# Kernel tuning notes

Measured on AMD Instinct MI355X. Metric: run time of the kernel, lower is better.

The kernel has to match this reference:

```python
import jax, jax.numpy as jnp
import numpy as np

H = 100
N = 262144

def setup_inputs() -> dict:
    key = jax.random.key(0)
    ks = jax.random.split(key, 9)
    s = 1.0 / np.sqrt(H)
    return {
        "m": jax.random.normal(ks[0], (1, H), jnp.float32),
        "output_hidden": jax.random.normal(ks[1], (1, 1, H), jnp.float32),
        "fact_embeddings": jax.random.normal(ks[2], (N, H), jnp.float32),
        "W1": jax.random.normal(ks[3], (H, 2 * H), jnp.float32) * s,
        "b1": jax.random.normal(ks[4], (H,), jnp.float32) * s,
        "W2": jax.random.normal(ks[5], (1, H), jnp.float32) * s,
        "b2": jax.random.normal(ks[6], (1,), jnp.float32) * s,
        "W3": jax.random.normal(ks[7], (H, 3 * H), jnp.float32) * s,
        "b3": jax.random.normal(ks[8], (H,), jnp.float32) * s,
    }

def reference(m, output_hidden, fact_embeddings, W1, b1, W2, b2, W3, b3):
    output_context = output_hidden[0]                      # [1, H]
    # z = [|f - oh| ; |f - m|]  -> [N, 2H] (broadcast over N)
    z = jnp.concatenate(
        [jnp.abs(fact_embeddings - output_context),
         jnp.abs(fact_embeddings - m)], axis=1)
    # MLP attention scores, softmax over N facts
    g = jnp.tanh(z @ W1.T + b1) @ W2.T + b2                # [N, 1]
    g = jax.nn.softmax(g.ravel())                          # [N]
    # Weighted-sum pooling of facts
    c = (g[:, None] * fact_embeddings).sum(axis=0, keepdims=True)  # [1, H]
    # Gated memory update
    m_new = jax.nn.relu(jnp.concatenate([m, c, output_context], axis=1) @ W3.T + b3)
    return m_new
```

## Files before the change

kernel.cpp:

```cpp
#include <hip/hip_runtime.h>
#include <hip/hip_bf16.h>
#include <math.h>

#define HDIM 100
#define NFACT 262144
#define FPB   128
#define NBLK_T 2048
#define TPB   4
#define GRID  (NBLK_T / TPB)
#define NTHREADS 512

#define KHALF 112
#define NJT 7
#define NKC 7
#define NBFRAG (NJT * NKC * 64)

#define NCOPY 116
#define NSTRIPE 4

using short8 = __attribute__((ext_vector_type(8))) short;
using f32x4  = __attribute__((ext_vector_type(4))) float;

#define WS_B    0
#define WS_ACC  12544

__device__ __forceinline__ unsigned short f2bf(float x) {
    unsigned u = __builtin_bit_cast(unsigned, x);
    u += 0x7FFFu + ((u >> 16) & 1u);
    return (unsigned short)(u >> 16);
}

__device__ __forceinline__ float tanh_fast(float x) {
    float e = __expf(2.0f * x);
    return 1.0f - 2.0f / (1.0f + e);
}

__global__ __launch_bounds__(256) void k_prep_b(const float* __restrict__ W1,
                                                float* __restrict__ ws) {
    int tg = blockIdx.x * 256 + threadIdx.x;
    if (tg < NSTRIPE * NCOPY) ws[WS_ACC + tg] = 0.f;
    if (tg >= NBFRAG) return;
    int lane = tg & 63;
    int kc = (tg >> 6) % NKC;
    int jt = tg / (NKC * 64);
    int g = lane >> 4, r = lane & 15;
    int j = jt * 16 + r;
    unsigned short v[8];
    #pragma unroll
    for (int e = 0; e < 8; e++) {
        int kglob = kc * 32 + g * 8 + e;
        int half = (kglob >= KHALF) ? 1 : 0;
        int koff = kglob - half * KHALF;
        float x = 0.f;
        if (j < HDIM && koff < HDIM) x = W1[j * 200 + half * HDIM + koff];
        v[e] = f2bf(x);
    }
    uint4 d;
    d.x = (unsigned)v[0] | ((unsigned)v[1] << 16);
    d.y = (unsigned)v[2] | ((unsigned)v[3] << 16);
    d.z = (unsigned)v[4] | ((unsigned)v[5] << 16);
    d.w = (unsigned)v[6] | ((unsigned)v[7] << 16);
    ((uint4*)(ws + WS_B))[tg] = d;
}

__device__ __forceinline__ float4 ld4c(const float* p, bool ok) {
    float4 z = make_float4(0.f, 0.f, 0.f, 0.f);
    return ok ? *(const float4*)p : z;
}

__device__ __forceinline__ uint4 pack_absdiff_u(float4 a0, float4 a1,
                                                float4 b0, float4 b1) {
    union { __hip_bfloat16 h[8]; uint4 u; } u;
    u.h[0] = __float2bfloat16(fabsf(a0.x - b0.x));
    u.h[1] = __float2bfloat16(fabsf(a0.y - b0.y));
    u.h[2] = __float2bfloat16(fabsf(a0.z - b0.z));
    u.h[3] = __float2bfloat16(fabsf(a0.w - b0.w));
    u.h[4] = __float2bfloat16(fabsf(a1.x - b1.x));
    u.h[5] = __float2bfloat16(fabsf(a1.y - b1.y));
    u.h[6] = __float2bfloat16(fabsf(a1.z - b1.z));
    u.h[7] = __float2bfloat16(fabsf(a1.w - b1.w));
    return u.u;
}

__device__ __forceinline__ float4 shfl32_f4(float4 v) {
    float4 r;
    r.x = __shfl_xor(v.x, 32); r.y = __shfl_xor(v.y, 32);
    r.z = __shfl_xor(v.z, 32); r.w = __shfl_xor(v.w, 32);
    return r;
}

template<int CTRL>
__device__ __forceinline__ float dpp_radd(float x) {
    int y = __builtin_amdgcn_update_dpp(0, __builtin_bit_cast(int, x),
                                        CTRL, 0xF, 0xF, true);
    return x + __builtin_bit_cast(float, y);
}
__device__ __forceinline__ float row_reduce16(float x) {
    x = dpp_radd<0x121>(x);
    x = dpp_radd<0x122>(x);
    x = dpp_radd<0x124>(x);
    x = dpp_radd<0x128>(x);
    return x;
}

__global__ __launch_bounds__(NTHREADS, 2) void k_logits(
        const float* __restrict__ fe,
        const float* __restrict__ oc,
        const float* __restrict__ mvec,
        const float* __restrict__ b1,
        const float* __restrict__ W2,
        float* __restrict__ ws) {
    __shared__ __align__(16) uint4 Bs[NBFRAG];
    __shared__ float poolS[KHALF];
    __shared__ float cpad[2 * KHALF];
    __shared__ float bw[2 * KHALF];
    __shared__ float sS;

    int t = threadIdx.x;
    int w = t >> 6, lane = t & 63, g = lane >> 4, r = lane & 15;
    bool ghi = (lane & 32) != 0;

    if (t == 0) sS = 0.f;
    if (t < KHALF) poolS[t] = 0.f;

    if (t < 2 * KHALF) {
        int half = t / KHALF, k = t % KHALF;
        cpad[t] = (k < HDIM) ? (half ? mvec[k] : oc[k]) : 0.f;
        bw[t]   = (k < HDIM) ? (half ? W2[k]   : b1[k]) : 0.f;
    }

    {
        const uint4* Bg = (const uint4*)(ws + WS_B);
        #pragma unroll
        for (int i = 0; i < 7; i++) {
            int base = i * 512 + w * 64;
            if (base < NBFRAG) {
                __builtin_amdgcn_global_load_lds(
                    (const __attribute__((address_space(1))) unsigned int*)(Bg + base + lane),
                    (__attribute__((address_space(3))) unsigned int*)(Bs + base),
                    16, 0, 0);
            }
        }
    }

    int row_off = w * 16 + r;

    auto issue_load = [&](int tile, float4* f0, float4* f1) {
        const float* fp = fe + ((long)tile * FPB + row_off) * HDIM;
        if (tile != NBLK_T - 1) {
            #pragma unroll
            for (int kc = 0; kc < 4; kc++) {
                int pk = kc * 32 + g * 8;
                int col = (pk >= KHALF) ? (pk - KHALF) : pk;
                f0[kc] = *(const float4*)(fp + col);
                f1[kc] = *(const float4*)(fp + col + 4);
            }
        } else {
            #pragma unroll
            for (int kc = 0; kc < 4; kc++) {
                int pk = kc * 32 + g * 8;
                int col = (pk >= KHALF) ? (pk - KHALF) : pk;
                f0[kc] = ld4c(fp + col, col < HDIM);
                f1[kc] = ld4c(fp + col + 4, col + 4 < HDIM);
            }
        }
    };

    float sacc = 0.f;

    auto process = [&](float4* f0c, float4* f1c) {
        uint4 zabs[NKC];
        #pragma unroll
        for (int kc = 0; kc < 4; kc++) {
            int pk = kc * 32 + g * 8;
            float4 s0 = *(const float4*)(cpad + pk);
            float4 s1 = *(const float4*)(cpad + pk + 4);
            zabs[kc] = pack_absdiff_u(f0c[kc], f1c[kc], s0, s1);
        }
        #pragma unroll
        for (int c = 0; c < 3; c++) {
            int pk = (4 + c) * 32 + g * 8;
            float4 sa0 = ghi ? f0c[c] : f0c[c + 1];
            float4 sa1 = ghi ? f1c[c] : f1c[c + 1];
            float4 ra0 = shfl32_f4(sa0);
            float4 ra1 = shfl32_f4(sa1);
            float4 s0 = *(const float4*)(cpad + pk);
            float4 s1 = *(const float4*)(cpad + pk + 4);
            zabs[4 + c] = pack_absdiff_u(ra0, ra1, s0, s1);
        }

        float gacc = 0.f;
        #pragma unroll
        for (int jt = 0; jt < NJT; jt++) {
            int jb = jt * 16 + g * 4;
            float4 b1q = *(const float4*)(bw + jb);
            float4 w2q = *(const float4*)(bw + KHALF + jb);
            f32x4 acc = {b1q.x, b1q.y, b1q.z, b1q.w};
            #pragma unroll
            for (int kc = 0; kc < NKC; kc++) {
                short8 av = __builtin_bit_cast(short8, Bs[(jt * NKC + kc) * 64 + lane]);
                acc = __builtin_amdgcn_mfma_f32_16x16x32_bf16(
                    av, __builtin_bit_cast(short8, zabs[kc]), acc, 0, 0, 0);
            }
            gacc = fmaf(tanh_fast(acc[0]), w2q.x, gacc);
            gacc = fmaf(tanh_fast(acc[1]), w2q.y, gacc);
            gacc = fmaf(tanh_fast(acc[2]), w2q.z, gacc);
            gacc = fmaf(tanh_fast(acc[3]), w2q.w, gacc);
        }
        gacc += __shfl_xor(gacc, 16);
        gacc += __shfl_xor(gacc, 32);
        float w_r = __expf(gacc);
        sacc += w_r;

        float p[4][8];
        #pragma unroll
        for (int c = 0; c < 4; c++) {
            p[c][0] = w_r * f0c[c].x; p[c][1] = w_r * f0c[c].y;
            p[c][2] = w_r * f0c[c].z; p[c][3] = w_r * f0c[c].w;
            p[c][4] = w_r * f1c[c].x; p[c][5] = w_r * f1c[c].y;
            p[c][6] = w_r * f1c[c].z; p[c][7] = w_r * f1c[c].w;
        }
        #pragma unroll
        for (int c = 0; c < 4; c++)
            #pragma unroll
            for (int e = 0; e < 8; e++) p[c][e] = row_reduce16(p[c][e]);
        if (r == 0) {
            #pragma unroll
            for (int c = 0; c < 4; c++) {
                int pk = c * 32 + g * 8;
                if (pk < KHALF) {
                    #pragma unroll
                    for (int e = 0; e < 8; e++)
                        atomicAdd(&poolS[pk + e], p[c][e]);
                }
            }
        }
    };

    int tile0 = blockIdx.x * TPB;
    float4 fA0[4], fA1[4], fB0[4], fB1[4];

    issue_load(tile0 + 0, fA0, fA1);
    __syncthreads();

    issue_load(tile0 + 1, fB0, fB1);
    process(fA0, fA1);
    __builtin_amdgcn_sched_barrier(0);

    issue_load(tile0 + 2, fA0, fA1);
    process(fB0, fB1);
    __builtin_amdgcn_sched_barrier(0);

    issue_load(tile0 + 3, fB0, fB1);
    process(fA0, fA1);
    __builtin_amdgcn_sched_barrier(0);

    process(fB0, fB1);

    float s16 = row_reduce16(sacc);
    if (lane == 0) atomicAdd(&sS, s16);
    __syncthreads();

    int cp = (blockIdx.x & (NSTRIPE - 1)) * NCOPY;
    if (t < KHALF && t < HDIM) atomicAdd(&ws[WS_ACC + cp + t], poolS[t]);
    if (t == 0) atomicAdd(&ws[WS_ACC + cp + KHALF], sS);
}

__global__ __launch_bounds__(128) void k_final(
        const float* __restrict__ mvec,
        const float* __restrict__ oc,
        const float* __restrict__ W3,
        const float* __restrict__ b3,
        const float* __restrict__ ws,
        float* __restrict__ out) {
    __shared__ float vv[300];
    int t = threadIdx.x;
    float S = 0.f;
    #pragma unroll
    for (int i = 0; i < NSTRIPE; i++) S += ws[WS_ACC + i * NCOPY + KHALF];
    if (t < HDIM) {
        float corr = 0.f;
        #pragma unroll
        for (int i = 0; i < NSTRIPE; i++) corr += ws[WS_ACC + i * NCOPY + t];
        vv[t] = mvec[t];
        vv[HDIM + t] = corr / S;
        vv[2 * HDIM + t] = oc[t];
    }
    __syncthreads();
    if (t < HDIM) {
        float a = b3[t];
        const float* wr = W3 + t * 3 * HDIM;
        #pragma unroll 4
        for (int k = 0; k < 3 * HDIM; k++) a = fmaf(wr[k], vv[k], a);
        out[t] = fmaxf(a, 0.f);
    }
}

extern "C" void kernel_launch(void* const* d_in, const int* in_sizes, int n_in,
                              void* d_out, int out_size, void* d_ws, size_t ws_size,
                              hipStream_t stream) {
    const float* mvec = (const float*)d_in[0];
    const float* oh   = (const float*)d_in[1];
    const float* fe   = (const float*)d_in[2];
    const float* W1   = (const float*)d_in[3];
    const float* b1   = (const float*)d_in[4];
    const float* W2   = (const float*)d_in[5];
    const float* W3   = (const float*)d_in[7];
    const float* b3   = (const float*)d_in[8];
    float* ws  = (float*)d_ws;
    float* out = (float*)d_out;

    k_prep_b<<<13, 256, 0, stream>>>(W1, ws);
    k_logits<<<GRID, NTHREADS, 0, stream>>>(fe, oh, mvec, b1, W2, ws);
    k_final<<<1, 128, 0, stream>>>(mvec, oh, W3, b3, ws, out);
}
```

Measured before the change: 74.89 us.

## Fuse final gated update into logits kernel via last-block ticket

Result: slower. 117.3 us (+56.6%).

```diff
diff --git a/kernel.cpp b/kernel.cpp
--- a/kernel.cpp
+++ b/kernel.cpp
@@ -21,8 +21,9 @@
 using short8 = __attribute__((ext_vector_type(8))) short;
 using f32x4  = __attribute__((ext_vector_type(4))) float;
 
-#define WS_B    0
-#define WS_ACC  12544
+#define WS_B      0
+#define WS_ACC    12544
+#define WS_TICKET (WS_ACC + NSTRIPE * NCOPY)
 
 __device__ __forceinline__ unsigned short f2bf(float x) {
     unsigned u = __builtin_bit_cast(unsigned, x);
@@ -38,7 +39,7 @@
 __global__ __launch_bounds__(256) void k_prep_b(const float* __restrict__ W1,
                                                 float* __restrict__ ws) {
     int tg = blockIdx.x * 256 + threadIdx.x;
-    if (tg < NSTRIPE * NCOPY) ws[WS_ACC + tg] = 0.f;
+    if (tg < NSTRIPE * NCOPY + 1) ws[WS_ACC + tg] = 0.f;
     if (tg >= NBFRAG) return;
     int lane = tg & 63;
     int kc = (tg >> 6) % NKC;
@@ -103,18 +104,26 @@
     return x;
 }
 
+__device__ __forceinline__ float agent_load(const float* p) {
+    return __hip_atomic_load(p, __ATOMIC_RELAXED, __HIP_MEMORY_SCOPE_AGENT);
+}
+
 __global__ __launch_bounds__(NTHREADS, 2) void k_logits(
         const float* __restrict__ fe,
         const float* __restrict__ oc,
         const float* __restrict__ mvec,
         const float* __restrict__ b1,
         const float* __restrict__ W2,
+        const float* __restrict__ W3,
+        const float* __restrict__ b3,
+        float* __restrict__ out,
         float* __restrict__ ws) {
     __shared__ __align__(16) uint4 Bs[NBFRAG];
     __shared__ float poolS[KHALF];
     __shared__ float cpad[2 * KHALF];
     __shared__ float bw[2 * KHALF];
     __shared__ float sS;
+    __shared__ unsigned lastFlag;
 
     int t = threadIdx.x;
     int w = t >> 6, lane = t & 63, g = lane >> 4, r = lane & 15;
@@ -264,34 +273,53 @@
     int cp = (blockIdx.x & (NSTRIPE - 1)) * NCOPY;
     if (t < KHALF && t < HDIM) atomicAdd(&ws[WS_ACC + cp + t], poolS[t]);
     if (t == 0) atomicAdd(&ws[WS_ACC + cp + KHALF], sS);
-}
-
-__global__ __launch_bounds__(128) void k_final(
-        const float* __restrict__ mvec,
-        const float* __restrict__ oc,
-        const float* __restrict__ W3,
-        const float* __restrict__ b3,
-        const float* __restrict__ ws,
-        float* __restrict__ out) {
-    __shared__ float vv[300];
-    int t = threadIdx.x;
-    float S = 0.f;
-    #pragma unroll
-    for (int i = 0; i < NSTRIPE; i++) S += ws[WS_ACC + i * NCOPY + KHALF];
+
+    __threadfence();
+    if (t == 0) {
+        unsigned old = atomicAdd((unsigned*)(ws + WS_TICKET), 1u);
+        lastFlag = (old == GRID - 1) ? 1u : 0u;
+    }
+    __syncthreads();
+    if (!lastFlag) return;
+
+    float* vv   = (float*)Bs;
+    float* part = (float*)Bs + 512;
+    __shared__ float Sval;
+
+    if (t == 0) {
+        float S = 0.f;
+        #pragma unroll
+        for (int i = 0; i < NSTRIPE; i++)
+            S += agent_load(&ws[WS_ACC + i * NCOPY + KHALF]);
+        Sval = S;
+    }
     if (t < HDIM) {
         float corr = 0.f;
         #pragma unroll
-        for (int i = 0; i < NSTRIPE; i++) corr += ws[WS_ACC + i * NCOPY + t];
+        for (int i = 0; i < NSTRIPE; i++)
+            corr += agent_load(&ws[WS_ACC + i * NCOPY + t]);
+        vv[HDIM + t] = corr;
         vv[t] = mvec[t];
-        vv[HDIM + t] = corr / S;
         vv[2 * HDIM + t] = oc[t];
+    }
+    __syncthreads();
+    if (t < HDIM) vv[HDIM + t] = vv[HDIM + t] / Sval;
+    __syncthreads();
+
+    if (t < 500) {
+        int sl = t / HDIM, h = t % HDIM;
+        const float* wr = W3 + h * 3 * HDIM + sl * 60;
+        const float* vp = vv + sl * 60;
+        float a = 0.f;
+        #pragma unroll 4
+        for (int k = 0; k < 60; k++) a = fmaf(wr[k], vp[k], a);
+        part[sl * HDIM + h] = a;
     }
     __syncthreads();
     if (t < HDIM) {
         float a = b3[t];
-        const float* wr = W3 + t * 3 * HDIM;
-        #pragma unroll 4
-        for (int k = 0; k < 3 * HDIM; k++) a = fmaf(wr[k], vv[k], a);
+        #pragma unroll
+        for (int sl = 0; sl < 5; sl++) a += part[sl * HDIM + t];
         out[t] = fmaxf(a, 0.f);
     }
 }
@@ -311,6 +339,5 @@
     float* out = (float*)d_out;
 
     k_prep_b<<<13, 256, 0, stream>>>(W1, ws);
-    k_logits<<<GRID, NTHREADS, 0, stream>>>(fe, oh, mvec, b1, W2, ws);
-    k_final<<<1, 128, 0, stream>>>(mvec, oh, W3, b3, ws, out);
-}
+    k_logits<<<GRID, NTHREADS, 0, stream>>>(fe, oh, mvec, b1, W2, W3, b3, out, ws);
+}
```
